# Kernel tuning notes

Hardware: AMD Instinct MI355X
Metric: run time of the kernel (lower is better)

## Reference

```python
import jax, jax.numpy as jnp
import numpy as np

BS, N, DIM, HEADS = 4, 2048, 512, 8
HEAD_DIM = DIM // HEADS
SCALE = HEAD_DIM ** 0.5
NEG = -1000000.0


def setup_inputs() -> dict:
    key = jax.random.key(0)
    ks = jax.random.split(key, 6)
    x = jax.random.normal(ks[0], (BS, N, DIM), dtype=jnp.float32)
    mask = jax.random.randint(ks[1], (BS, N), 0, 2, dtype=jnp.int32)
    s = 1.0 / np.sqrt(DIM)
    Wq = jax.random.normal(ks[2], (DIM, DIM), dtype=jnp.float32) * s
    Wk = jax.random.normal(ks[3], (DIM, DIM), dtype=jnp.float32) * s
    Wv = jax.random.normal(ks[4], (DIM, DIM), dtype=jnp.float32) * s
    Wo = jax.random.normal(ks[5], (DIM, DIM), dtype=jnp.float32) * s
    return {"x": x, "Wq": Wq, "Wk": Wk, "Wv": Wv, "Wo": Wo, "mask": mask}


def reference(x, Wq, Wk, Wv, Wo, mask):
    # q,k,v: (bs, n, dim) -> (bs, h, n, d)
    def split_heads(t):
        return t.reshape(BS, N, HEADS, HEAD_DIM).transpose(0, 2, 1, 3)
    q = split_heads(x @ Wq.T)
    k = split_heads(x @ Wk.T)
    v = split_heads(x @ Wv.T)
    # scores: (bs, h, n, n)
    scores = jnp.einsum('bhqd,bhkd->bhqk', q, k) / SCALE
    # key-padding mask broadcast over heads and query positions
    keep = (mask == 1)[:, None, None, :]  # (bs,1,1,n)
    scores = jnp.where(keep, scores, NEG)
    attn = jax.nn.softmax(scores, axis=-1)
    out = jnp.einsum('bhqk,bhkd->bhqd', attn, v)
    out = out.transpose(0, 2, 1, 3).reshape(BS, N, DIM)
    return out @ Wo.T
```

## Files before the change

### kernel.cpp

```cpp
#include <hip/hip_runtime.h>
#include <hip/hip_bf16.h>

#define BS 4
#define SEQ 2048
#define DIM 512
#define HEADS 8
#define HD 64
#define ROWS (BS*SEQ)
#define SCL2E 0.1803368801111244f
#define NEGB (-1.4426950408889634e6f)

typedef __attribute__((ext_vector_type(8))) short bf16x8;
typedef __attribute__((ext_vector_type(4))) short bf16x4;
typedef __attribute__((ext_vector_type(4))) float floatx4;
typedef unsigned short u16;
typedef unsigned int u32;

#if defined(__has_builtin)
# if __has_builtin(__builtin_amdgcn_mfma_f32_16x16x16bf16_1k)
#  define HAVE_MFMA16 1
# endif
#endif
#ifndef HAVE_MFMA16
# define HAVE_MFMA16 0
#endif

__device__ __forceinline__ u16 f2bf(float f) {
    union { float f; unsigned u; } v; v.f = f;
    unsigned r = v.u + 0x7fff + ((v.u >> 16) & 1);
    return (u16)(r >> 16);
}

__device__ __forceinline__ unsigned pack2bf(float a, float b) {
#if __has_builtin(__builtin_amdgcn_cvt_pk_bf16_f32)
    typedef __attribute__((ext_vector_type(2))) __bf16 bf2;
    union { bf2 v; unsigned u; } cv;
    cv.v = __builtin_amdgcn_cvt_pk_bf16_f32(a, b);
    return cv.u;
#else
    return (unsigned)f2bf(a) | ((unsigned)f2bf(b) << 16);
#endif
}

__device__ __forceinline__ float fexp2(float x) {
#if __has_builtin(__builtin_amdgcn_exp2f)
    return __builtin_amdgcn_exp2f(x);
#else
    return __expf(x * 0.6931471805599453f);
#endif
}

__device__ __forceinline__ void gload16(const u16* g, u16* l) {
    __builtin_amdgcn_global_load_lds(
        (const __attribute__((address_space(1))) u32*)g,
        (__attribute__((address_space(3))) u32*)l, 16, 0, 0);
}

__global__ __launch_bounds__(256) void convert_all(
    const float* __restrict__ x, const float* __restrict__ Wq,
    const float* __restrict__ Wk, const float* __restrict__ Wv,
    const float* __restrict__ Wo, const int* __restrict__ mask,
    u16* __restrict__ xb, u16* __restrict__ wqb,
    u16* __restrict__ wkb, u16* __restrict__ wvb,
    u16* __restrict__ wob, float* __restrict__ biasf)
{
    int i = blockIdx.x * 256 + threadIdx.x;
    if (i < 1048576 + 262144) {
        const float* src; u16* dst; int off;
        if (i < 1048576) { src = x; dst = xb; off = i; }
        else {
            int j = i - 1048576; int seg = j >> 16; off = j & 65535;
            src = seg == 0 ? Wq : seg == 1 ? Wk : seg == 2 ? Wv : Wo;
            dst = seg == 0 ? wqb : seg == 1 ? wkb : seg == 2 ? wvb : wob;
        }
        float4 v = ((const float4*)src)[off];
        ushort4 o;
        o.x = f2bf(v.x); o.y = f2bf(v.y); o.z = f2bf(v.z); o.w = f2bf(v.w);
        ((ushort4*)dst)[off] = o;
    } else {
        int jb = i - 1310720;
        int4 mv = ((const int4*)mask)[jb];
        float4 bo;
        bo.x = (mv.x == 1) ? 0.f : NEGB;
        bo.y = (mv.y == 1) ? 0.f : NEGB;
        bo.z = (mv.z == 1) ? 0.f : NEGB;
        bo.w = (mv.w == 1) ? 0.f : NEGB;
        ((float4*)biasf)[jb] = bo;
    }
}

__global__ __launch_bounds__(256, 3) void gemm_qkv_fused(
    const u16* __restrict__ A, const u16* __restrict__ Wcat,
    u16* __restrict__ Oq, u16* __restrict__ Okf, u16* __restrict__ Ovf)
{
    __shared__ u16 ldsA[8192];
    __shared__ u16 ldsB[8192];

    int n0 = blockIdx.x * 128;
    int m0 = blockIdx.y * 128;
    int tid = threadIdx.x;
    int w = tid >> 6, lane = tid & 63, quad = lane >> 4, l16 = lane & 15;
    int mo = (w & 1) * 64, no = (w >> 1) * 64;
    int l7 = l16 & 7;

    int sr = lane >> 3, sc = lane & 7, gc = sc ^ sr;
    const u16* gA0 = A    + (long)(m0 + sr) * DIM + gc * 8;
    const u16* gB0 = Wcat + (long)(n0 + sr) * DIM + gc * 8;

    floatx4 acc[4][4];
    #pragma unroll
    for (int mt = 0; mt < 4; mt++)
        #pragma unroll
        for (int nt = 0; nt < 4; nt++) acc[mt][nt] = (floatx4){0.f,0.f,0.f,0.f};

    for (int k0 = 0; k0 < DIM; k0 += 64) {
        #pragma unroll
        for (int i = 0; i < 4; i++) {
            int ch = w * 4 + i;
            gload16(gA0 + (long)ch * 8 * DIM + k0, &ldsA[ch * 512]);
            gload16(gB0 + (long)ch * 8 * DIM + k0, &ldsB[ch * 512]);
        }
        __syncthreads();

        #pragma unroll
        for (int kc = 0; kc < 2; kc++) {
            int swz = ((kc * 4 + quad) ^ l7) * 8;
            bf16x8 af[4], bf[4];
            #pragma unroll
            for (int t4 = 0; t4 < 4; t4++) {
                af[t4] = *(const bf16x8*)&ldsA[(mo + t4*16 + l16) * 64 + swz];
                bf[t4] = *(const bf16x8*)&ldsB[(no + t4*16 + l16) * 64 + swz];
            }
            #pragma unroll
            for (int mt = 0; mt < 4; mt++)
                #pragma unroll
                for (int nt = 0; nt < 4; nt++)
                    acc[mt][nt] = __builtin_amdgcn_mfma_f32_16x16x32_bf16(
                        af[mt], bf[nt], acc[mt][nt], 0, 0, 0);
        }
        __syncthreads();
    }

    int seg = n0 >> 9;
    if (seg == 0) {
        #pragma unroll
        for (int mt = 0; mt < 4; mt++)
            #pragma unroll
            for (int nt = 0; nt < 4; nt++)
                #pragma unroll
                for (int r = 0; r < 4; r++) {
                    int row = m0 + mo + mt*16 + quad*4 + r;
                    int col9 = (n0 + no + nt*16 + l16) & 511;
                    int b = row >> 11, n = row & 2047, h = col9 >> 6, d = col9 & 63;
                    Oq[(((long)(b * HEADS + h) * SEQ + n) << 6) + d] = f2bf(acc[mt][nt][r]);
                }
    } else if (seg == 1) {
        #pragma unroll
        for (int mt = 0; mt < 4; mt++)
            #pragma unroll
            for (int nt = 0; nt < 4; nt++)
                #pragma unroll
                for (int r = 0; r < 4; r++) {
                    int row = m0 + mo + mt*16 + quad*4 + r;
                    int col9 = (n0 + no + nt*16 + l16) & 511;
                    int b = row >> 11, keyn = row & 2047, h = col9 >> 6, dd = col9 & 63;
                    int kt = keyn >> 6, ntk = (keyn >> 4) & 3, l16k = keyn & 15;
                    int g = dd >> 5, quadk = (dd >> 3) & 3, j = dd & 7;
                    long offv = ((long)((b*HEADS + h)*32 + kt) << 12)
                              + ((ntk*2 + g) << 9) + ((quadk*16 + l16k) << 3) + j;
                    Okf[offv] = f2bf(acc[mt][nt][r] * SCL2E);
                }
    } else {
#if HAVE_MFMA16
        #pragma unroll
        for (int mt = 0; mt < 4; mt++)
            #pragma unroll
            for (int nt = 0; nt < 4; nt++) {
                int rowb = m0 + mo + mt*16 + quad*4;
                int col9 = (n0 + no + nt*16 + l16) & 511;
                int b = rowb >> 11, keyn = rowb & 2047, h = col9 >> 6, dd = col9 & 63;
                int kt = keyn >> 6;
                int wf = (keyn >> 4) & 3, quadf = (keyn >> 2) & 3;
                int ctf = dd >> 4, l16f = dd & 15;
                long offv = ((long)((b*HEADS + h)*32 + kt) << 12)
                          + (wf << 10) + ((quadf*16 + l16f) << 4) + (ctf << 2);
                ushort4 st;
                st.x = f2bf(acc[mt][nt][0]); st.y = f2bf(acc[mt][nt][1]);
                st.z = f2bf(acc[mt][nt][2]); st.w = f2bf(acc[mt][nt][3]);
                *(ushort4*)&Ovf[offv] = st;
            }
#else
        #pragma unroll
        for (int mt = 0; mt < 4; mt++)
            #pragma unroll
            for (int nt = 0; nt < 4; nt++) {
                int rowb = m0 + mo + mt*16 + quad*4;
                int col9 = (n0 + no + nt*16 + l16) & 511;
                int b = rowb >> 11, keyn = rowb & 2047, h = col9 >> 6, dd = col9 & 63;
                int kt = keyn >> 6, g = (keyn >> 5) & 1, quadv = (keyn >> 3) & 3, jk = keyn & 7;
                int ctv = dd >> 4, l16v = dd & 15;
                long offv = ((long)((b*HEADS + h)*32 + kt) << 12)
                          + ((ctv*2 + g) << 9) + ((quadv*16 + l16v) << 3) + jk;
                ushort4 st;
                st.x = f2bf(acc[mt][nt][0]); st.y = f2bf(acc[mt][nt][1]);
                st.z = f2bf(acc[mt][nt][2]); st.w = f2bf(acc[mt][nt][3]);
                *(ushort4*)&Ovf[offv] = st;
            }
#endif
    }
}

#if HAVE_MFMA16
__global__ __launch_bounds__(256, 3) void flash_attn(
    const u16* __restrict__ Q, const u16* __restrict__ Kf,
    const u16* __restrict__ Vf, const float* __restrict__ biasf,
    u16* __restrict__ ctx)
{
    __shared__ float red[4352];

    int bx = blockIdx.x;
    int c  = bx & 7, s = bx >> 3;
    int g  = ((s >> 5) << 3) | c;
    int i  = s & 31;
    int q0 = i * 64;
    int h  = g & 7;
    int b  = g >> 3;
    int bh = b * HEADS + h;

    int tid = threadIdx.x;
    int w = tid >> 6, lane = tid & 63, quad = lane >> 4, l16 = lane & 15;

    bf16x8 qb[4][2];
    #pragma unroll
    for (int nt = 0; nt < 4; nt++) {
        const u16* qp = Q + ((long)bh * SEQ + q0 + nt*16 + l16) * HD + quad * 8;
        qb[nt][0] = *(const bf16x8*)(qp);
        qb[nt][1] = *(const bf16x8*)(qp + 32);
    }

    const u16* Kbh = Kf + ((long)bh << 17) + w*1024 + lane*8;
    const u16* Vbh = Vf + ((long)bh << 17) + w*1024 + lane*16;
    const float* bb = biasf + b * SEQ + w*16 + quad*4;

    short one_s = (l16 == 0) ? (short)0x3F80 : (short)0;
    bf16x4 onesb = { one_s, one_s, one_s, one_s };

    bf16x8 ka0 = *(const bf16x8*)(Kbh);
    bf16x8 ka1 = *(const bf16x8*)(Kbh + 512);
    bf16x8 vlo = *(const bf16x8*)(Vbh);
    bf16x8 vhi = *(const bf16x8*)(Vbh + 8);
    float4 bv  = *(const float4*)(bb);

    floatx4 o[4][4];
    floatx4 o5[4];
    #pragma unroll
    for (int nt = 0; nt < 4; nt++) {
        #pragma unroll
        for (int ct = 0; ct < 4; ct++) o[nt][ct] = (floatx4){0.f,0.f,0.f,0.f};
        o5[nt] = (floatx4){0.f,0.f,0.f,0.f};
    }

    #pragma unroll 2
    for (int t = 0; t < 32; t++) {
        bf16x8 ka0n = ka0, ka1n = ka1, vlon = vlo, vhin = vhi;
        float4 bvn = bv;
        if (t < 31) {
            const u16* kp = Kbh + (long)(t+1)*4096;
            const u16* vp = Vbh + (long)(t+1)*4096;
            ka0n = *(const bf16x8*)(kp);
            ka1n = *(const bf16x8*)(kp + 512);
            vlon = *(const bf16x8*)(vp);
            vhin = *(const bf16x8*)(vp + 8);
            bvn  = *(const float4*)(bb + (t+1)*64);
        }

        union { bf16x8 v8; bf16x4 v4[2]; } uvl, uvh;
        uvl.v8 = vlo; uvh.v8 = vhi;
        bf16x4 vb[4] = { uvl.v4[0], uvl.v4[1], uvh.v4[0], uvh.v4[1] };

        #pragma unroll
        for (int nt = 0; nt < 4; nt++) {
            floatx4 s2;
            s2[0] = bv.x; s2[1] = bv.y; s2[2] = bv.z; s2[3] = bv.w;
            s2 = __builtin_amdgcn_mfma_f32_16x16x32_bf16(ka0, qb[nt][0], s2, 0, 0, 0);
            s2 = __builtin_amdgcn_mfma_f32_16x16x32_bf16(ka1, qb[nt][1], s2, 0, 0, 0);
            float p0 = fexp2(s2[0]);
            float p1 = fexp2(s2[1]);
            float p2 = fexp2(s2[2]);
            float p3 = fexp2(s2[3]);
            union { bf16x4 v; unsigned u[2]; } pu;
            pu.u[0] = pack2bf(p0, p1);
            pu.u[1] = pack2bf(p2, p3);
            #pragma unroll
            for (int ct = 0; ct < 4; ct++)
                o[nt][ct] = __builtin_amdgcn_mfma_f32_16x16x16bf16_1k(
                    pu.v, vb[ct], o[nt][ct], 0, 0, 0);
            o5[nt] = __builtin_amdgcn_mfma_f32_16x16x16bf16_1k(
                pu.v, onesb, o5[nt], 0, 0, 0);
        }

        ka0 = ka0n; ka1 = ka1n; vlo = vlon; vhi = vhin; bv = bvn;
    }

    __syncthreads();
    float* ldsf = red;
    floatx4* ldsv = (floatx4*)red;

    if (l16 == 0) {
        #pragma unroll
        for (int nt = 0; nt < 4; nt++)
            #pragma unroll
            for (int r = 0; r < 4; r++)
                ldsf[4096 + w*64 + nt*16 + quad*4 + r] = o5[nt][r];
    }
    __syncthreads();

    #pragma unroll
    for (int i2 = 1; i2 < 4; i2++) {
        int tslot = (w + i2) & 3;
        #pragma unroll
        for (int nt = 0; nt < 4; nt++)
            if (nt == tslot) {
                #pragma unroll
                for (int ct = 0; ct < 4; ct++)
                    ldsv[nt*256 + ct*64 + lane] = o[nt][ct];
            }
        __syncthreads();
        #pragma unroll
        for (int nt = 0; nt < 4; nt++)
            if (nt == w) {
                #pragma unroll
                for (int ct = 0; ct < 4; ct++) {
                    floatx4 v = ldsv[nt*256 + ct*64 + lane];
                    o[nt][ct] += v;
                }
            }
        __syncthreads();
    }

    #pragma unroll
    for (int nt = 0; nt < 4; nt++) {
        if (nt != w) continue;
        float inv[4];
        #pragma unroll
        for (int r = 0; r < 4; r++) {
            int q = w*16 + quad*4 + r;
            float sden = ldsf[4096 + q] + ldsf[4096 + 64 + q]
                       + ldsf[4096 + 128 + q] + ldsf[4096 + 192 + q];
            inv[r] = 1.0f / sden;
        }
        #pragma unroll
        for (int ct = 0; ct < 4; ct++) {
            int col = h * HD + ct*16 + l16;
            long rb = (long)(b * SEQ + q0 + w*16 + quad*4);
            #pragma unroll
            for (int r = 0; r < 4; r++)
                ctx[(rb + r) * DIM + col] = f2bf(o[nt][ct][r] * inv[r]);
        }
    }
}
#else
__global__ __launch_bounds__(256, 4) void flash_attn(
    const u16* __restrict__ Q, const u16* __restrict__ Kf,
    const u16* __restrict__ Vf, const float* __restrict__ biasf,
    u16* __restrict__ ctx)
{
    __shared__ u16 lds[20480];

    int bx = blockIdx.x;
    int q0 = (bx & 31) * 64;
    int h  = (bx >> 5) & 7;
    int b  = bx >> 8;
    int bh = b * HEADS + h;

    int tid = threadIdx.x;
    int w = tid >> 6, lane = tid & 63, quad = lane >> 4, l16 = lane & 15;

    const u16* Qp = Q + ((long)bh * SEQ + q0 + w*16 + l16) * HD + quad * 8;
    bf16x8 qb0 = *(const bf16x8*)(Qp);
    bf16x8 qb1 = *(const bf16x8*)(Qp + 32);

    const u16* Kbh = Kf + ((long)bh << 17);
    const u16* Vbh = Vf + ((long)bh << 17);
    const float* bbase = biasf + b * SEQ + quad * 4;

    u16* Prow = &lds[16384 + w * 1024 + l16 * 64];
    int swz = l16 & 7;

    {
        const u16* gk = Kbh + (2*w)*512 + lane*8;
        const u16* gv = Vbh + (2*w)*512 + lane*8;
        gload16(gk,       &lds[(2*w)*512]);
        gload16(gk + 512, &lds[(2*w+1)*512]);
        gload16(gv,       &lds[8192 + (2*w)*512]);
        gload16(gv + 512, &lds[8192 + (2*w+1)*512]);
    }
    __syncthreads();

    floatx4 o[4];
    #pragma unroll
    for (int ct = 0; ct < 4; ct++) o[ct] = (floatx4){0.f, 0.f, 0.f, 0.f};
    float lsum = 0.f;

    for (int t = 0; t < 32; t++) {
        int cur = t & 1;
        if (t < 31) {
            long tb = (long)(t + 1) << 12;
            int nb = cur ^ 1;
            const u16* gk = Kbh + tb + (2*w)*512 + lane*8;
            const u16* gv = Vbh + tb + (2*w)*512 + lane*8;
            gload16(gk,       &lds[nb*4096 + (2*w)*512]);
            gload16(gk + 512, &lds[nb*4096 + (2*w+1)*512]);
            gload16(gv,       &lds[8192 + nb*4096 + (2*w)*512]);
            gload16(gv + 512, &lds[8192 + nb*4096 + (2*w+1)*512]);
        }

        const u16* Kl = &lds[cur * 4096];
        const u16* Vl = &lds[8192 + cur * 4096];

        #pragma unroll
        for (int nt = 0; nt < 4; nt++) {
            float4 bv = *(const float4*)(bbase + t*64 + nt*16);
            bf16x8 ka0 = *(const bf16x8*)(Kl + (nt*2 + 0)*512 + lane*8);
            bf16x8 ka1 = *(const bf16x8*)(Kl + (nt*2 + 1)*512 + lane*8);
            floatx4 tt;
            tt[0] = bv.x; tt[1] = bv.y; tt[2] = bv.z; tt[3] = bv.w;
            tt = __builtin_amdgcn_mfma_f32_16x16x32_bf16(ka0, qb0, tt, 0, 0, 0);
            tt = __builtin_amdgcn_mfma_f32_16x16x32_bf16(ka1, qb1, tt, 0, 0, 0);
            float p0 = fexp2(tt[0]);
            float p1 = fexp2(tt[1]);
            float p2 = fexp2(tt[2]);
            float p3 = fexp2(tt[3]);
            lsum += (p0 + p1) + (p2 + p3);
            int gx = nt*2 + (quad >> 1);
            uint2 pu;
            pu.x = pack2bf(p0, p1);
            pu.y = pack2bf(p2, p3);
            *(uint2*)(Prow + ((gx ^ swz) << 3) + (quad & 1)*4) = pu;
        }

        #pragma unroll
        for (int g = 0; g < 2; g++) {
            bf16x8 pa = *(const bf16x8*)(Prow + (((g*4 + quad) ^ swz) << 3));
            #pragma unroll
            for (int ct = 0; ct < 4; ct++) {
                bf16x8 vbf = *(const bf16x8*)(Vl + (ct*2 + g)*512 + lane*8);
                o[ct] = __builtin_amdgcn_mfma_f32_16x16x32_bf16(pa, vbf, o[ct], 0, 0, 0);
            }
        }

        __syncthreads();
    }

    lsum += __shfl_xor(lsum, 16);
    lsum += __shfl_xor(lsum, 32);
    float inv = 1.0f / lsum;
    float i0 = __shfl(inv, quad*4 + 0);
    float i1 = __shfl(inv, quad*4 + 1);
    float i2 = __shfl(inv, quad*4 + 2);
    float i3 = __shfl(inv, quad*4 + 3);
    #pragma unroll
    for (int ct = 0; ct < 4; ct++) {
        int col = h * HD + ct*16 + l16;
        long rb = (long)(b * SEQ + q0 + w*16 + quad*4);
        ctx[(rb + 0) * DIM + col] = f2bf(o[ct][0] * i0);
        ctx[(rb + 1) * DIM + col] = f2bf(o[ct][1] * i1);
        ctx[(rb + 2) * DIM + col] = f2bf(o[ct][2] * i2);
        ctx[(rb + 3) * DIM + col] = f2bf(o[ct][3] * i3);
    }
}
#endif

__global__ __launch_bounds__(256, 4) void gemm_proj(
    const u16* __restrict__ A, const u16* __restrict__ Bt,
    float* __restrict__ Out)
{
    __shared__ u16 ldsA[4096];
    __shared__ u16 ldsB[8192];

    int n0 = blockIdx.x * 128;
    int m0 = blockIdx.y * 64;
    int tid = threadIdx.x;
    int w = tid >> 6, lane = tid & 63, quad = lane >> 4, l16 = lane & 15;
    int l7 = l16 & 7;

    int sr = lane >> 3, sc = lane & 7, gc = sc ^ sr;
    const u16* gA0 = A  + (long)(m0 + sr) * DIM + gc * 8;
    const u16* gB0 = Bt + (long)(n0 + sr) * DIM + gc * 8;

    floatx4 acc[8];
    #pragma unroll
    for (int nt = 0; nt < 8; nt++) acc[nt] = (floatx4){0.f,0.f,0.f,0.f};

    for (int k0 = 0; k0 < DIM; k0 += 64) {
        gload16(gA0 + (long)(2*w)   * 8 * DIM + k0, &ldsA[(2*w)   * 512]);
        gload16(gA0 + (long)(2*w+1) * 8 * DIM + k0, &ldsA[(2*w+1) * 512]);
        #pragma unroll
        for (int i = 0; i < 4; i++)
            gload16(gB0 + (long)(4*w+i) * 8 * DIM + k0, &ldsB[(4*w+i) * 512]);
        __syncthreads();

        #pragma unroll
        for (int kc = 0; kc < 2; kc++) {
            int swz = ((kc * 4 + quad) ^ l7) * 8;
            bf16x8 af = *(const bf16x8*)&ldsA[(w*16 + l16) * 64 + swz];
            #pragma unroll
            for (int nt = 0; nt < 8; nt++) {
                bf16x8 bfv = *(const bf16x8*)&ldsB[(nt*16 + l16) * 64 + swz];
                acc[nt] = __builtin_amdgcn_mfma_f32_16x16x32_bf16(
                    af, bfv, acc[nt], 0, 0, 0);
            }
        }
        __syncthreads();
    }

    #pragma unroll
    for (int nt = 0; nt < 8; nt++)
        #pragma unroll
        for (int r = 0; r < 4; r++) {
            int row = m0 + w*16 + quad*4 + r;
            int col = n0 + nt*16 + l16;
            Out[(long)row * DIM + col] = acc[nt][r];
        }
}

extern "C" void kernel_launch(void* const* d_in, const int* in_sizes, int n_in,
                              void* d_out, int out_size, void* d_ws, size_t ws_size,
                              hipStream_t stream) {
    const float* x  = (const float*)d_in[0];
    const float* Wq = (const float*)d_in[1];
    const float* Wk = (const float*)d_in[2];
    const float* Wv = (const float*)d_in[3];
    const float* Wo = (const float*)d_in[4];
    const int* mask = (const int*)d_in[5];
    float* out = (float*)d_out;

    char* ws = (char*)d_ws;
    size_t off = 0;
    u16* xb  = (u16*)(ws + off); off += (size_t)ROWS * DIM * 2;
    u16* wqb = (u16*)(ws + off); off += (size_t)DIM * DIM * 2;
    u16* wkb = (u16*)(ws + off); off += (size_t)DIM * DIM * 2;
    u16* wvb = (u16*)(ws + off); off += (size_t)DIM * DIM * 2;
    u16* wob = (u16*)(ws + off); off += (size_t)DIM * DIM * 2;
    u16* Qh  = (u16*)(ws + off); off += (size_t)ROWS * DIM * 2;
    u16* Kfr = (u16*)(ws + off); off += (size_t)ROWS * DIM * 2;
    u16* Vfr = (u16*)(ws + off); off += (size_t)ROWS * DIM * 2;
    u16* ctx = (u16*)(ws + off); off += (size_t)ROWS * DIM * 2;
    float* biasf = (float*)(ws + off); off += (size_t)BS * SEQ * 4;

    convert_all<<<5128, 256, 0, stream>>>(x, Wq, Wk, Wv, Wo, mask,
                                          xb, wqb, wkb, wvb, wob, biasf);
    gemm_qkv_fused<<<dim3(12, 64), 256, 0, stream>>>(xb, wqb, Qh, Kfr, Vfr);
    flash_attn<<<BS * HEADS * (SEQ / 64), 256, 0, stream>>>(Qh, Kfr, Vfr, biasf, ctx);
    gemm_proj<<<dim3(4, 128), 256, 0, stream>>>(ctx, wob, out);

    (void)in_sizes; (void)n_in; (void)out_size; (void)ws_size;
}
```

Baseline: 156.5 us.

## Process two key tiles per iteration using 16x16x32 MFMA for PV

The attention loop now handles two 16-key sub-tiles per wave per iteration. The probability fragments are packed into 8-wide bf16 vectors so the P·V and row-sum products use the K=32 MFMA instead of two K=16 MFMAs. This halves the number of PV MFMA instructions and loop iterations, and it doubles the prefetch depth per iteration. In exchange it raises register pressure, so launch bounds drop from 3 to 2 waves-per-SIMD occupancy, and the new V element ordering must match the stored V layout.

```diff
diff --git a/kernel.cpp b/kernel.cpp
--- a/kernel.cpp
+++ b/kernel.cpp
@@ -211,7 +211,7 @@
 }
 
 #if HAVE_MFMA16
-__global__ __launch_bounds__(256, 3) void flash_attn(
+__global__ __launch_bounds__(256, 2) void flash_attn(
     const u16* __restrict__ Q, const u16* __restrict__ Kf,
     const u16* __restrict__ Vf, const float* __restrict__ biasf,
     u16* __restrict__ ctx)
@@ -238,18 +238,23 @@
         qb[nt][1] = *(const bf16x8*)(qp + 32);
     }
 
-    const u16* Kbh = Kf + ((long)bh << 17) + w*1024 + lane*8;
-    const u16* Vbh = Vf + ((long)bh << 17) + w*1024 + lane*16;
-    const float* bb = biasf + b * SEQ + w*16 + quad*4;
+    const u16* Kw = Kf + ((long)bh << 17) + w*2048 + lane*8;
+    const u16* Vw = Vf + ((long)bh << 17) + w*2048 + lane*16;
+    const float* bw = biasf + b * SEQ + w*32 + quad*4;
 
     short one_s = (l16 == 0) ? (short)0x3F80 : (short)0;
-    bf16x4 onesb = { one_s, one_s, one_s, one_s };
-
-    bf16x8 ka0 = *(const bf16x8*)(Kbh);
-    bf16x8 ka1 = *(const bf16x8*)(Kbh + 512);
-    bf16x8 vlo = *(const bf16x8*)(Vbh);
-    bf16x8 vhi = *(const bf16x8*)(Vbh + 8);
-    float4 bv  = *(const float4*)(bb);
+    bf16x8 ones8 = { one_s, one_s, one_s, one_s, one_s, one_s, one_s, one_s };
+
+    bf16x8 k00 = *(const bf16x8*)(Kw);
+    bf16x8 k01 = *(const bf16x8*)(Kw + 512);
+    bf16x8 k10 = *(const bf16x8*)(Kw + 1024);
+    bf16x8 k11 = *(const bf16x8*)(Kw + 1536);
+    bf16x8 v0l = *(const bf16x8*)(Vw);
+    bf16x8 v0h = *(const bf16x8*)(Vw + 8);
+    bf16x8 v1l = *(const bf16x8*)(Vw + 1024);
+    bf16x8 v1h = *(const bf16x8*)(Vw + 1032);
+    float4 bv0 = *(const float4*)(bw);
+    float4 bv1 = *(const float4*)(bw + 16);
 
     floatx4 o[4][4];
     floatx4 o5[4];
@@ -260,46 +265,69 @@
         o5[nt] = (floatx4){0.f,0.f,0.f,0.f};
     }
 
+    union U8 { bf16x8 v8; bf16x4 v4[2]; };
+
     #pragma unroll 2
-    for (int t = 0; t < 32; t++) {
-        bf16x8 ka0n = ka0, ka1n = ka1, vlon = vlo, vhin = vhi;
-        float4 bvn = bv;
-        if (t < 31) {
-            const u16* kp = Kbh + (long)(t+1)*4096;
-            const u16* vp = Vbh + (long)(t+1)*4096;
-            ka0n = *(const bf16x8*)(kp);
-            ka1n = *(const bf16x8*)(kp + 512);
-            vlon = *(const bf16x8*)(vp);
-            vhin = *(const bf16x8*)(vp + 8);
-            bvn  = *(const float4*)(bb + (t+1)*64);
-        }
-
-        union { bf16x8 v8; bf16x4 v4[2]; } uvl, uvh;
-        uvl.v8 = vlo; uvh.v8 = vhi;
-        bf16x4 vb[4] = { uvl.v4[0], uvl.v4[1], uvh.v4[0], uvh.v4[1] };
+    for (int it = 0; it < 16; it++) {
+        bf16x8 k00n=k00, k01n=k01, k10n=k10, k11n=k11;
+        bf16x8 v0ln=v0l, v0hn=v0h, v1ln=v1l, v1hn=v1h;
+        float4 bv0n=bv0, bv1n=bv1;
+        if (it < 15) {
+            const u16* kp = Kw + (long)(it+1)*8192;
+            const u16* vp = Vw + (long)(it+1)*8192;
+            k00n = *(const bf16x8*)(kp);
+            k01n = *(const bf16x8*)(kp + 512);
+            k10n = *(const bf16x8*)(kp + 1024);
+            k11n = *(const bf16x8*)(kp + 1536);
+            v0ln = *(const bf16x8*)(vp);
+            v0hn = *(const bf16x8*)(vp + 8);
+            v1ln = *(const bf16x8*)(vp + 1024);
+            v1hn = *(const bf16x8*)(vp + 1032);
+            bv0n = *(const float4*)(bw + (it+1)*128);
+            bv1n = *(const float4*)(bw + (it+1)*128 + 16);
+        }
+
+        U8 a0, a1, b0, b1;
+        a0.v8 = v0l; a1.v8 = v0h; b0.v8 = v1l; b1.v8 = v1h;
+        U8 vb[4];
+        vb[0].v4[0] = a0.v4[0]; vb[0].v4[1] = b0.v4[0];
+        vb[1].v4[0] = a0.v4[1]; vb[1].v4[1] = b0.v4[1];
+        vb[2].v4[0] = a1.v4[0]; vb[2].v4[1] = b1.v4[0];
+        vb[3].v4[0] = a1.v4[1]; vb[3].v4[1] = b1.v4[1];
 
         #pragma unroll
         for (int nt = 0; nt < 4; nt++) {
-            floatx4 s2;
-            s2[0] = bv.x; s2[1] = bv.y; s2[2] = bv.z; s2[3] = bv.w;
-            s2 = __builtin_amdgcn_mfma_f32_16x16x32_bf16(ka0, qb[nt][0], s2, 0, 0, 0);
-            s2 = __builtin_amdgcn_mfma_f32_16x16x32_bf16(ka1, qb[nt][1], s2, 0, 0, 0);
-            float p0 = fexp2(s2[0]);
-            float p1 = fexp2(s2[1]);
-            float p2 = fexp2(s2[2]);
-            float p3 = fexp2(s2[3]);
-            union { bf16x4 v; unsigned u[2]; } pu;
-            pu.u[0] = pack2bf(p0, p1);
-            pu.u[1] = pack2bf(p2, p3);
+            floatx4 s0, s1;
+            s0[0] = bv0.x; s0[1] = bv0.y; s0[2] = bv0.z; s0[3] = bv0.w;
+            s1[0] = bv1.x; s1[1] = bv1.y; s1[2] = bv1.z; s1[3] = bv1.w;
+            s0 = __builtin_amdgcn_mfma_f32_16x16x32_bf16(k00, qb[nt][0], s0, 0, 0, 0);
+            s0 = __builtin_amdgcn_mfma_f32_16x16x32_bf16(k01, qb[nt][1], s0, 0, 0, 0);
+            s1 = __builtin_amdgcn_mfma_f32_16x16x32_bf16(k10, qb[nt][0], s1, 0, 0, 0);
+            s1 = __builtin_amdgcn_mfma_f32_16x16x32_bf16(k11, qb[nt][1], s1, 0, 0, 0);
+            float pA0 = fexp2(s0[0]);
+            float pA1 = fexp2(s0[1]);
+            float pA2 = fexp2(s0[2]);
+            float pA3 = fexp2(s0[3]);
+            float pB0 = fexp2(s1[0]);
+            float pB1 = fexp2(s1[1]);
+            float pB2 = fexp2(s1[2]);
+            float pB3 = fexp2(s1[3]);
+            union { bf16x8 v; unsigned u[4]; } pu;
+            pu.u[0] = pack2bf(pA0, pA1);
+            pu.u[1] = pack2bf(pA2, pA3);
+            pu.u[2] = pack2bf(pB0, pB1);
+            pu.u[3] = pack2bf(pB2, pB3);
             #pragma unroll
             for (int ct = 0; ct < 4; ct++)
-                o[nt][ct] = __builtin_amdgcn_mfma_f32_16x16x16bf16_1k(
-                    pu.v, vb[ct], o[nt][ct], 0, 0, 0);
-            o5[nt] = __builtin_amdgcn_mfma_f32_16x16x16bf16_1k(
-                pu.v, onesb, o5[nt], 0, 0, 0);
-        }
-
-        ka0 = ka0n; ka1 = ka1n; vlo = vlon; vhi = vhin; bv = bvn;
+                o[nt][ct] = __builtin_amdgcn_mfma_f32_16x16x32_bf16(
+                    pu.v, vb[ct].v8, o[nt][ct], 0, 0, 0);
+            o5[nt] = __builtin_amdgcn_mfma_f32_16x16x32_bf16(
+                pu.v, ones8, o5[nt], 0, 0, 0);
+        }
+
+        k00 = k00n; k01 = k01n; k10 = k10n; k11 = k11n;
+        v0l = v0ln; v0h = v0hn; v1l = v1ln; v1h = v1hn;
+        bv0 = bv0n; bv1 = bv1n;
     }
 
     __syncthreads();
```

Measured after the change: 158.2 us. Within noise of the previous version (+1.1%).

## Split attention waves into 2x2 query/key groups with K=32 PV MFMAs

Applied to the files above, without the earlier changes.

The flash attention kernel now partitions its four waves as two query groups by two key halves instead of each wave owning a 16-key slice for all 64 queries. Each wave computes 32 queries against 32 keys per tile, so the PV product uses 16x16x32 MFMAs rather than 16x16x16. The V projection output layout changes to match. The cross-wave reduction at the end shrinks from a three-round four-way exchange to a single pairwise LDS exchange with one barrier. It also drops the non-MFMA16 fallback paths; the cost is more K/V registers per wave and different load patterns.

```diff
diff --git a/kernel.cpp b/kernel.cpp
--- a/kernel.cpp
+++ b/kernel.cpp
@@ -15,15 +15,6 @@
 typedef __attribute__((ext_vector_type(4))) float floatx4;
 typedef unsigned short u16;
 typedef unsigned int u32;
-
-#if defined(__has_builtin)
-# if __has_builtin(__builtin_amdgcn_mfma_f32_16x16x16bf16_1k)
-#  define HAVE_MFMA16 1
-# endif
-#endif
-#ifndef HAVE_MFMA16
-# define HAVE_MFMA16 0
-#endif
 
 __device__ __forceinline__ u16 f2bf(float f) {
     union { float f; unsigned u; } v; v.f = f;
@@ -171,305 +162,204 @@
                     Okf[offv] = f2bf(acc[mt][nt][r] * SCL2E);
                 }
     } else {
-#if HAVE_MFMA16
         #pragma unroll
         for (int mt = 0; mt < 4; mt++)
             #pragma unroll
             for (int nt = 0; nt < 4; nt++) {
                 int rowb = m0 + mo + mt*16 + quad*4;
                 int col9 = (n0 + no + nt*16 + l16) & 511;
-                int b = rowb >> 11, keyn = rowb & 2047, h = col9 >> 6, dd = col9 & 63;
-                int kt = keyn >> 6;
-                int wf = (keyn >> 4) & 3, quadf = (keyn >> 2) & 3;
-                int ctf = dd >> 4, l16f = dd & 15;
-                long offv = ((long)((b*HEADS + h)*32 + kt) << 12)
-                          + (wf << 10) + ((quadf*16 + l16f) << 4) + (ctf << 2);
+                int b = rowb >> 11, keyn = rowb & 2047, h = col9 >> 6;
+                int tile = (keyn >> 6) & 31;
+                long offv = ((long)((b*HEADS + h)*32 + tile) << 12)
+                          + ((long)(mt >> 1) << 11) + (nt << 9)
+                          + ((quad*16 + l16) << 3) + ((mt & 1) << 2);
                 ushort4 st;
                 st.x = f2bf(acc[mt][nt][0]); st.y = f2bf(acc[mt][nt][1]);
                 st.z = f2bf(acc[mt][nt][2]); st.w = f2bf(acc[mt][nt][3]);
                 *(ushort4*)&Ovf[offv] = st;
             }
-#else
-        #pragma unroll
-        for (int mt = 0; mt < 4; mt++)
-            #pragma unroll
-            for (int nt = 0; nt < 4; nt++) {
-                int rowb = m0 + mo + mt*16 + quad*4;
-                int col9 = (n0 + no + nt*16 + l16) & 511;
-                int b = rowb >> 11, keyn = rowb & 2047, h = col9 >> 6, dd = col9 & 63;
-                int kt = keyn >> 6, g = (keyn >> 5) & 1, quadv = (keyn >> 3) & 3, jk = keyn & 7;
-                int ctv = dd >> 4, l16v = dd & 15;
-                long offv = ((long)((b*HEADS + h)*32 + kt) << 12)
-                          + ((ctv*2 + g) << 9) + ((quadv*16 + l16v) << 3) + jk;
-                ushort4 st;
-                st.x = f2bf(acc[mt][nt][0]); st.y = f2bf(acc[mt][nt][1]);
-                st.z = f2bf(acc[mt][nt][2]); st.w = f2bf(acc[mt][nt][3]);
-                *(ushort4*)&Ovf[offv] = st;
-            }
-#endif
-    }
-}
-
-#if HAVE_MFMA16
+    }
+}
+
 __global__ __launch_bounds__(256, 3) void flash_attn(
     const u16* __restrict__ Q, const u16* __restrict__ Kf,
     const u16* __restrict__ Vf, const float* __restrict__ biasf,
     u16* __restrict__ ctx)
 {
-    __shared__ float red[4352];
+    __shared__ float red[4224];
 
     int bx = blockIdx.x;
-    int c  = bx & 7, s = bx >> 3;
-    int g  = ((s >> 5) << 3) | c;
-    int i  = s & 31;
-    int q0 = i * 64;
-    int h  = g & 7;
-    int b  = g >> 3;
+    int cx = bx & 7, sx = bx >> 3;
+    int gg = ((sx >> 5) << 3) | cx;
+    int qi = sx & 31;
+    int q0 = qi * 64;
+    int h  = gg & 7;
+    int b  = gg >> 3;
     int bh = b * HEADS + h;
 
     int tid = threadIdx.x;
     int w = tid >> 6, lane = tid & 63, quad = lane >> 4, l16 = lane & 15;
-
-    bf16x8 qb[4][2];
-    #pragma unroll
-    for (int nt = 0; nt < 4; nt++) {
-        const u16* qp = Q + ((long)bh * SEQ + q0 + nt*16 + l16) * HD + quad * 8;
-        qb[nt][0] = *(const bf16x8*)(qp);
-        qb[nt][1] = *(const bf16x8*)(qp + 32);
-    }
-
-    const u16* Kbh = Kf + ((long)bh << 17) + w*1024 + lane*8;
-    const u16* Vbh = Vf + ((long)bh << 17) + w*1024 + lane*16;
-    const float* bb = biasf + b * SEQ + w*16 + quad*4;
+    int wq = w >> 1, wk = w & 1;
+
+    bf16x8 qA0, qA1, qB0, qB1;
+    {
+        const u16* qp = Q + ((long)bh * SEQ + q0 + wq*32 + l16) * HD + quad * 8;
+        qA0 = *(const bf16x8*)(qp);
+        qA1 = *(const bf16x8*)(qp + 32);
+        qB0 = *(const bf16x8*)(qp + 16*HD);
+        qB1 = *(const bf16x8*)(qp + 16*HD + 32);
+    }
+
+    const u16* Kw = Kf + ((long)bh << 17) + wk*2048 + lane*8;
+    const u16* Vw = Vf + ((long)bh << 17) + wk*2048 + lane*8;
+    const float* bw = biasf + b * SEQ + wk*32 + quad*4;
 
     short one_s = (l16 == 0) ? (short)0x3F80 : (short)0;
-    bf16x4 onesb = { one_s, one_s, one_s, one_s };
-
-    bf16x8 ka0 = *(const bf16x8*)(Kbh);
-    bf16x8 ka1 = *(const bf16x8*)(Kbh + 512);
-    bf16x8 vlo = *(const bf16x8*)(Vbh);
-    bf16x8 vhi = *(const bf16x8*)(Vbh + 8);
-    float4 bv  = *(const float4*)(bb);
-
-    floatx4 o[4][4];
-    floatx4 o5[4];
-    #pragma unroll
-    for (int nt = 0; nt < 4; nt++) {
-        #pragma unroll
-        for (int ct = 0; ct < 4; ct++) o[nt][ct] = (floatx4){0.f,0.f,0.f,0.f};
-        o5[nt] = (floatx4){0.f,0.f,0.f,0.f};
-    }
+    bf16x8 ones8 = { one_s, one_s, one_s, one_s, one_s, one_s, one_s, one_s };
+
+    bf16x8 kA0 = *(const bf16x8*)(Kw);
+    bf16x8 kA1 = *(const bf16x8*)(Kw + 512);
+    bf16x8 kB0 = *(const bf16x8*)(Kw + 1024);
+    bf16x8 kB1 = *(const bf16x8*)(Kw + 1536);
+    bf16x8 vb0 = *(const bf16x8*)(Vw);
+    bf16x8 vb1 = *(const bf16x8*)(Vw + 512);
+    bf16x8 vb2 = *(const bf16x8*)(Vw + 1024);
+    bf16x8 vb3 = *(const bf16x8*)(Vw + 1536);
+    float4 bv0 = *(const float4*)(bw);
+    float4 bv1 = *(const float4*)(bw + 16);
+
+    floatx4 oA[4], oB[4], o5A, o5B;
+    #pragma unroll
+    for (int ct = 0; ct < 4; ct++) {
+        oA[ct] = (floatx4){0.f,0.f,0.f,0.f};
+        oB[ct] = (floatx4){0.f,0.f,0.f,0.f};
+    }
+    o5A = (floatx4){0.f,0.f,0.f,0.f};
+    o5B = (floatx4){0.f,0.f,0.f,0.f};
 
     #pragma unroll 2
-    for (int t = 0; t < 32; t++) {
-        bf16x8 ka0n = ka0, ka1n = ka1, vlon = vlo, vhin = vhi;
-        float4 bvn = bv;
-        if (t < 31) {
-            const u16* kp = Kbh + (long)(t+1)*4096;
-            const u16* vp = Vbh + (long)(t+1)*4096;
-            ka0n = *(const bf16x8*)(kp);
-            ka1n = *(const bf16x8*)(kp + 512);
-            vlon = *(const bf16x8*)(vp);
-            vhin = *(const bf16x8*)(vp + 8);
-            bvn  = *(const float4*)(bb + (t+1)*64);
-        }
-
-        union { bf16x8 v8; bf16x4 v4[2]; } uvl, uvh;
-        uvl.v8 = vlo; uvh.v8 = vhi;
-        bf16x4 vb[4] = { uvl.v4[0], uvl.v4[1], uvh.v4[0], uvh.v4[1] };
-
-        #pragma unroll
-        for (int nt = 0; nt < 4; nt++) {
-            floatx4 s2;
-            s2[0] = bv.x; s2[1] = bv.y; s2[2] = bv.z; s2[3] = bv.w;
-            s2 = __builtin_amdgcn_mfma_f32_16x16x32_bf16(ka0, qb[nt][0], s2, 0, 0, 0);
-            s2 = __builtin_amdgcn_mfma_f32_16x16x32_bf16(ka1, qb[nt][1], s2, 0, 0, 0);
-            float p0 = fexp2(s2[0]);
-            float p1 = fexp2(s2[1]);
-            float p2 = fexp2(s2[2]);
-            float p3 = fexp2(s2[3]);
-            union { bf16x4 v; unsigned u[2]; } pu;
+    for (int it = 0; it < 32; it++) {
+        bf16x8 kA0n=kA0, kA1n=kA1, kB0n=kB0, kB1n=kB1;
+        bf16x8 vb0n=vb0, vb1n=vb1, vb2n=vb2, vb3n=vb3;
+        float4 bv0n=bv0, bv1n=bv1;
+        if (it < 31) {
+            const u16* kp = Kw + (long)(it+1)*4096;
+            const u16* vp = Vw + (long)(it+1)*4096;
+            kA0n = *(const bf16x8*)(kp);
+            kA1n = *(const bf16x8*)(kp + 512);
+            kB0n = *(const bf16x8*)(kp + 1024);
+            kB1n = *(const bf16x8*)(kp + 1536);
+            vb0n = *(const bf16x8*)(vp);
+            vb1n = *(const bf16x8*)(vp + 512);
+            vb2n = *(const bf16x8*)(vp + 1024);
+            vb3n = *(const bf16x8*)(vp + 1536);
+            bv0n = *(const float4*)(bw + (it+1)*64);
+            bv1n = *(const float4*)(bw + (it+1)*64 + 16);
+        }
+
+        {
+            floatx4 s0, s1;
+            s0[0] = bv0.x; s0[1] = bv0.y; s0[2] = bv0.z; s0[3] = bv0.w;
+            s1[0] = bv1.x; s1[1] = bv1.y; s1[2] = bv1.z; s1[3] = bv1.w;
+            s0 = __builtin_amdgcn_mfma_f32_16x16x32_bf16(kA0, qA0, s0, 0, 0, 0);
+            s0 = __builtin_amdgcn_mfma_f32_16x16x32_bf16(kA1, qA1, s0, 0, 0, 0);
+            s1 = __builtin_amdgcn_mfma_f32_16x16x32_bf16(kB0, qA0, s1, 0, 0, 0);
+            s1 = __builtin_amdgcn_mfma_f32_16x16x32_bf16(kB1, qA1, s1, 0, 0, 0);
+            float p0 = fexp2(s0[0]);
+            float p1 = fexp2(s0[1]);
+            float p2 = fexp2(s0[2]);
+            float p3 = fexp2(s0[3]);
+            float p4 = fexp2(s1[0]);
+            float p5 = fexp2(s1[1]);
+            float p6 = fexp2(s1[2]);
+            float p7 = fexp2(s1[3]);
+            union { bf16x8 v; unsigned u[4]; } pu;
             pu.u[0] = pack2bf(p0, p1);
             pu.u[1] = pack2bf(p2, p3);
-            #pragma unroll
-            for (int ct = 0; ct < 4; ct++)
-                o[nt][ct] = __builtin_amdgcn_mfma_f32_16x16x16bf16_1k(
-                    pu.v, vb[ct], o[nt][ct], 0, 0, 0);
-            o5[nt] = __builtin_amdgcn_mfma_f32_16x16x16bf16_1k(
-                pu.v, onesb, o5[nt], 0, 0, 0);
-        }
-
-        ka0 = ka0n; ka1 = ka1n; vlo = vlon; vhi = vhin; bv = bvn;
-    }
-
+            pu.u[2] = pack2bf(p4, p5);
+            pu.u[3] = pack2bf(p6, p7);
+            oA[0] = __builtin_amdgcn_mfma_f32_16x16x32_bf16(pu.v, vb0, oA[0], 0, 0, 0);
+            oA[1] = __builtin_amdgcn_mfma_f32_16x16x32_bf16(pu.v, vb1, oA[1], 0, 0, 0);
+            oA[2] = __builtin_amdgcn_mfma_f32_16x16x32_bf16(pu.v, vb2, oA[2], 0, 0, 0);
+            oA[3] = __builtin_amdgcn_mfma_f32_16x16x32_bf16(pu.v, vb3, oA[3], 0, 0, 0);
+            o5A  = __builtin_amdgcn_mfma_f32_16x16x32_bf16(pu.v, ones8, o5A, 0, 0, 0);
+        }
+        {
+            floatx4 s0, s1;
+            s0[0] = bv0.x; s0[1] = bv0.y; s0[2] = bv0.z; s0[3] = bv0.w;
+            s1[0] = bv1.x; s1[1] = bv1.y; s1[2] = bv1.z; s1[3] = bv1.w;
+            s0 = __builtin_amdgcn_mfma_f32_16x16x32_bf16(kA0, qB0, s0, 0, 0, 0);
+            s0 = __builtin_amdgcn_mfma_f32_16x16x32_bf16(kA1, qB1, s0, 0, 0, 0);
+            s1 = __builtin_amdgcn_mfma_f32_16x16x32_bf16(kB0, qB0, s1, 0, 0, 0);
+            s1 = __builtin_amdgcn_mfma_f32_16x16x32_bf16(kB1, qB1, s1, 0, 0, 0);
+            float p0 = fexp2(s0[0]);
+            float p1 = fexp2(s0[1]);
+            float p2 = fexp2(s0[2]);
+            float p3 = fexp2(s0[3]);
+            float p4 = fexp2(s1[0]);
+            float p5 = fexp2(s1[1]);
+            float p6 = fexp2(s1[2]);
+            float p7 = fexp2(s1[3]);
+            union { bf16x8 v; unsigned u[4]; } pu;
+            pu.u[0] = pack2bf(p0, p1);
+            pu.u[1] = pack2bf(p2, p3);
+            pu.u[2] = pack2bf(p4, p5);
+            pu.u[3] = pack2bf(p6, p7);
+            oB[0] = __builtin_amdgcn_mfma_f32_16x16x32_bf16(pu.v, vb0, oB[0], 0, 0, 0);
+            oB[1] = __builtin_amdgcn_mfma_f32_16x16x32_bf16(pu.v, vb1, oB[1], 0, 0, 0);
+            oB[2] = __builtin_amdgcn_mfma_f32_16x16x32_bf16(pu.v, vb2, oB[2], 0, 0, 0);
+            oB[3] = __builtin_amdgcn_mfma_f32_16x16x32_bf16(pu.v, vb3, oB[3], 0, 0, 0);
+            o5B  = __builtin_amdgcn_mfma_f32_16x16x32_bf16(pu.v, ones8, o5B, 0, 0, 0);
+        }
+
+        kA0 = kA0n; kA1 = kA1n; kB0 = kB0n; kB1 = kB1n;
+        vb0 = vb0n; vb1 = vb1n; vb2 = vb2n; vb3 = vb3n;
+        bv0 = bv0n; bv1 = bv1n;
+    }
+
+    floatx4* ldsv = (floatx4*)red;
+    float* ldsf = red;
+    int Town = wq*2 + wk;
+    int Tpar = wq*2 + (wk ^ 1);
+
+    if (wk == 0) {
+        #pragma unroll
+        for (int ct = 0; ct < 4; ct++)
+            ldsv[Tpar*256 + ct*64 + lane] = oB[ct];
+    } else {
+        #pragma unroll
+        for (int ct = 0; ct < 4; ct++)
+            ldsv[Tpar*256 + ct*64 + lane] = oA[ct];
+    }
+    if (l16 == 0) {
+        #pragma unroll
+        for (int r = 0; r < 4; r++) {
+            ldsf[4096 + ((wq*2 + 0)*2 + wk)*16 + quad*4 + r] = o5A[r];
+            ldsf[4096 + ((wq*2 + 1)*2 + wk)*16 + quad*4 + r] = o5B[r];
+        }
+    }
     __syncthreads();
-    float* ldsf = red;
-    floatx4* ldsv = (floatx4*)red;
-
-    if (l16 == 0) {
-        #pragma unroll
-        for (int nt = 0; nt < 4; nt++)
-            #pragma unroll
-            for (int r = 0; r < 4; r++)
-                ldsf[4096 + w*64 + nt*16 + quad*4 + r] = o5[nt][r];
-    }
-    __syncthreads();
-
-    #pragma unroll
-    for (int i2 = 1; i2 < 4; i2++) {
-        int tslot = (w + i2) & 3;
-        #pragma unroll
-        for (int nt = 0; nt < 4; nt++)
-            if (nt == tslot) {
-                #pragma unroll
-                for (int ct = 0; ct < 4; ct++)
-                    ldsv[nt*256 + ct*64 + lane] = o[nt][ct];
-            }
-        __syncthreads();
-        #pragma unroll
-        for (int nt = 0; nt < 4; nt++)
-            if (nt == w) {
-                #pragma unroll
-                for (int ct = 0; ct < 4; ct++) {
-                    floatx4 v = ldsv[nt*256 + ct*64 + lane];
-                    o[nt][ct] += v;
-                }
-            }
-        __syncthreads();
-    }
-
-    #pragma unroll
-    for (int nt = 0; nt < 4; nt++) {
-        if (nt != w) continue;
-        float inv[4];
-        #pragma unroll
-        for (int r = 0; r < 4; r++) {
-            int q = w*16 + quad*4 + r;
-            float sden = ldsf[4096 + q] + ldsf[4096 + 64 + q]
-                       + ldsf[4096 + 128 + q] + ldsf[4096 + 192 + q];
-            inv[r] = 1.0f / sden;
-        }
-        #pragma unroll
-        for (int ct = 0; ct < 4; ct++) {
-            int col = h * HD + ct*16 + l16;
-            long rb = (long)(b * SEQ + q0 + w*16 + quad*4);
-            #pragma unroll
-            for (int r = 0; r < 4; r++)
-                ctx[(rb + r) * DIM + col] = f2bf(o[nt][ct][r] * inv[r]);
-        }
-    }
-}
-#else
-__global__ __launch_bounds__(256, 4) void flash_attn(
-    const u16* __restrict__ Q, const u16* __restrict__ Kf,
-    const u16* __restrict__ Vf, const float* __restrict__ biasf,
-    u16* __restrict__ ctx)
-{
-    __shared__ u16 lds[20480];
-
-    int bx = blockIdx.x;
-    int q0 = (bx & 31) * 64;
-    int h  = (bx >> 5) & 7;
-    int b  = bx >> 8;
-    int bh = b * HEADS + h;
-
-    int tid = threadIdx.x;
-    int w = tid >> 6, lane = tid & 63, quad = lane >> 4, l16 = lane & 15;
-
-    const u16* Qp = Q + ((long)bh * SEQ + q0 + w*16 + l16) * HD + quad * 8;
-    bf16x8 qb0 = *(const bf16x8*)(Qp);
-    bf16x8 qb1 = *(const bf16x8*)(Qp + 32);
-
-    const u16* Kbh = Kf + ((long)bh << 17);
-    const u16* Vbh = Vf + ((long)bh << 17);
-    const float* bbase = biasf + b * SEQ + quad * 4;
-
-    u16* Prow = &lds[16384 + w * 1024 + l16 * 64];
-    int swz = l16 & 7;
-
-    {
-        const u16* gk = Kbh + (2*w)*512 + lane*8;
-        const u16* gv = Vbh + (2*w)*512 + lane*8;
-        gload16(gk,       &lds[(2*w)*512]);
-        gload16(gk + 512, &lds[(2*w+1)*512]);
-        gload16(gv,       &lds[8192 + (2*w)*512]);
-        gload16(gv + 512, &lds[8192 + (2*w+1)*512]);
-    }
-    __syncthreads();
-
-    floatx4 o[4];
-    #pragma unroll
-    for (int ct = 0; ct < 4; ct++) o[ct] = (floatx4){0.f, 0.f, 0.f, 0.f};
-    float lsum = 0.f;
-
-    for (int t = 0; t < 32; t++) {
-        int cur = t & 1;
-        if (t < 31) {
-            long tb = (long)(t + 1) << 12;
-            int nb = cur ^ 1;
-            const u16* gk = Kbh + tb + (2*w)*512 + lane*8;
-            const u16* gv = Vbh + tb + (2*w)*512 + lane*8;
-            gload16(gk,       &lds[nb*4096 + (2*w)*512]);
-            gload16(gk + 512, &lds[nb*4096 + (2*w+1)*512]);
-            gload16(gv,       &lds[8192 + nb*4096 + (2*w)*512]);
-            gload16(gv + 512, &lds[8192 + nb*4096 + (2*w+1)*512]);
-        }
-
-        const u16* Kl = &lds[cur * 4096];
-        const u16* Vl = &lds[8192 + cur * 4096];
-
-        #pragma unroll
-        for (int nt = 0; nt < 4; nt++) {
-            float4 bv = *(const float4*)(bbase + t*64 + nt*16);
-            bf16x8 ka0 = *(const bf16x8*)(Kl + (nt*2 + 0)*512 + lane*8);
-            bf16x8 ka1 = *(const bf16x8*)(Kl + (nt*2 + 1)*512 + lane*8);
-            floatx4 tt;
-            tt[0] = bv.x; tt[1] = bv.y; tt[2] = bv.z; tt[3] = bv.w;
-            tt = __builtin_amdgcn_mfma_f32_16x16x32_bf16(ka0, qb0, tt, 0, 0, 0);
-            tt = __builtin_amdgcn_mfma_f32_16x16x32_bf16(ka1, qb1, tt, 0, 0, 0);
-            float p0 = fexp2(tt[0]);
-            float p1 = fexp2(tt[1]);
-            float p2 = fexp2(tt[2]);
-            float p3 = fexp2(tt[3]);
-            lsum += (p0 + p1) + (p2 + p3);
-            int gx = nt*2 + (quad >> 1);
-            uint2 pu;
-            pu.x = pack2bf(p0, p1);
-            pu.y = pack2bf(p2, p3);
-            *(uint2*)(Prow + ((gx ^ swz) << 3) + (quad & 1)*4) = pu;
-        }
-
-        #pragma unroll
-        for (int g = 0; g < 2; g++) {
-            bf16x8 pa = *(const bf16x8*)(Prow + (((g*4 + quad) ^ swz) << 3));
-            #pragma unroll
-            for (int ct = 0; ct < 4; ct++) {
-                bf16x8 vbf = *(const bf16x8*)(Vl + (ct*2 + g)*512 + lane*8);
-                o[ct] = __builtin_amdgcn_mfma_f32_16x16x32_bf16(pa, vbf, o[ct], 0, 0, 0);
-            }
-        }
-
-        __syncthreads();
-    }
-
-    lsum += __shfl_xor(lsum, 16);
-    lsum += __shfl_xor(lsum, 32);
-    float inv = 1.0f / lsum;
-    float i0 = __shfl(inv, quad*4 + 0);
-    float i1 = __shfl(inv, quad*4 + 1);
-    float i2 = __shfl(inv, quad*4 + 2);
-    float i3 = __shfl(inv, quad*4 + 3);
+
+    float inv[4];
+    #pragma unroll
+    for (int r = 0; r < 4; r++) {
+        float sden = ldsf[4096 + (Town*2 + 0)*16 + quad*4 + r]
+                   + ldsf[4096 + (Town*2 + 1)*16 + quad*4 + r];
+        inv[r] = 1.0f / sden;
+    }
+
     #pragma unroll
     for (int ct = 0; ct < 4; ct++) {
+        floatx4 part = ldsv[Town*256 + ct*64 + lane];
+        floatx4 of = (wk == 0) ? oA[ct] : oB[ct];
+        of += part;
         int col = h * HD + ct*16 + l16;
-        long rb = (long)(b * SEQ + q0 + w*16 + quad*4);
-        ctx[(rb + 0) * DIM + col] = f2bf(o[ct][0] * i0);
-        ctx[(rb + 1) * DIM + col] = f2bf(o[ct][1] * i1);
-        ctx[(rb + 2) * DIM + col] = f2bf(o[ct][2] * i2);
-        ctx[(rb + 3) * DIM + col] = f2bf(o[ct][3] * i3);
-    }
-}
-#endif
+        long rb = (long)(b * SEQ + q0 + Town*16 + quad*4);
+        #pragma unroll
+        for (int r = 0; r < 4; r++)
+            ctx[(rb + r) * DIM + col] = f2bf(of[r] * inv[r]);
+    }
+}
 
 __global__ __launch_bounds__(256, 4) void gemm_proj(
     const u16* __restrict__ A, const u16* __restrict__ Bt,
```

After: 165.3 us. 5.6% more time.
